# Performance work log

Hardware: AMD Instinct MI355X
Metric: run time of the kernel (lower is better)

Reference implementation:

```python
import jax, jax.numpy as jnp
import numpy as np

N, E, D = 100000, 640000, 128  # nodes, edges, feature dim (in_dim == out_dim == 128)
BN_EPS = 1e-5


def setup_inputs() -> dict:
    key = jax.random.key(0)
    ks = jax.random.split(key, 8)
    x = jax.random.normal(ks[0], (N, D), dtype=jnp.float32)
    edge_index = jax.random.randint(ks[1], (2, E), 0, N, dtype=jnp.int64)
    s = 1.0 / np.sqrt(D)
    W1 = jax.random.uniform(ks[2], (D, D), jnp.float32, -s, s)
    b1 = jax.random.uniform(ks[3], (D,), jnp.float32, -s, s)
    W2 = jax.random.uniform(ks[4], (D, D), jnp.float32, -s, s)
    b2 = jax.random.uniform(ks[5], (D,), jnp.float32, -s, s)
    return {
        "x": x,
        "edge_index": edge_index,
        "eps": jnp.array([0.1], dtype=jnp.float32),
        "W1": W1, "b1": b1,
        "g1": jnp.ones((D,), jnp.float32), "beta1": jnp.zeros((D,), jnp.float32),
        "W2": W2, "b2": b2,
        "g2": jnp.ones((D,), jnp.float32), "beta2": jnp.zeros((D,), jnp.float32),
    }


def _batchnorm(h, gamma, beta):
    # BatchNorm1d in training mode: biased batch stats over the node dim
    mean = jnp.mean(h, axis=0)
    var = jnp.var(h, axis=0)
    return gamma * (h - mean) * jax.lax.rsqrt(var + BN_EPS) + beta


def reference(x, edge_index, eps, W1, b1, g1, beta1, W2, b2, g2, beta2):
    src, dst = edge_index[0], edge_index[1]
    # gather messages from source nodes, scatter-add into destination nodes
    aggr = jax.ops.segment_sum(x[src], dst, num_segments=x.shape[0])  # [N, D]
    h = (1.0 + eps) * x + aggr
    h = jax.nn.relu(_batchnorm(h @ W1.T + b1, g1, beta1))
    h = jax.nn.relu(_batchnorm(h @ W2.T + b2, g2, beta2))
    return h
```

## Files before the change

kernel.cpp:

```cpp
#include <hip/hip_runtime.h>

#define NN 100000
#define DD 128
#define EE 640000
#define NPAD 100352

typedef __bf16 bf16x8 __attribute__((ext_vector_type(8)));
typedef float floatx4 __attribute__((ext_vector_type(4)));

__device__ __forceinline__ unsigned short f2bf(float f) {
    unsigned int u = __float_as_uint(f);
    u += 0x7FFF + ((u >> 16) & 1);
    return (unsigned short)(u >> 16);
}

__global__ __launch_bounds__(256) void hist_k(const int* __restrict__ ei,
                                              int* __restrict__ deg) {
    int e = blockIdx.x * 256 + threadIdx.x;
    if (e < EE) atomicAdd(&deg[ei[EE + e]], 1);
}

__global__ __launch_bounds__(256) void scan1_k(const int* __restrict__ deg,
                                               int* __restrict__ exc,
                                               int* __restrict__ chunkSums) {
    __shared__ int s[256];
    int t = threadIdx.x, g = blockIdx.x * 256 + t;
    int v = (g < NN) ? deg[g] : 0;
    s[t] = v;
    __syncthreads();
    for (int off = 1; off < 256; off <<= 1) {
        int u = (t >= off) ? s[t - off] : 0;
        __syncthreads();
        s[t] += u;
        __syncthreads();
    }
    if (g < NN) exc[g] = s[t] - v;
    if (t == 255) chunkSums[blockIdx.x] = s[255];
}

__global__ __launch_bounds__(512) void scan2_k(int* __restrict__ chunkSums, int n) {
    __shared__ int s[512];
    int t = threadIdx.x;
    int v = (t < n) ? chunkSums[t] : 0;
    s[t] = v;
    __syncthreads();
    for (int off = 1; off < 512; off <<= 1) {
        int u = (t >= off) ? s[t - off] : 0;
        __syncthreads();
        s[t] += u;
        __syncthreads();
    }
    if (t < n) chunkSums[t] = s[t] - v;
}

__global__ __launch_bounds__(256) void scan3_k(int* __restrict__ exc,
                                               const int* __restrict__ chunkSums,
                                               int* __restrict__ cursor) {
    int g = blockIdx.x * 256 + threadIdx.x;
    if (g < NN) {
        int o = exc[g] + chunkSums[blockIdx.x];
        exc[g] = o;
        cursor[g] = o;
    }
}

__global__ __launch_bounds__(256) void esort_k(const int* __restrict__ ei,
                                               int* __restrict__ cursor,
                                               int* __restrict__ ssrc) {
    int e = blockIdx.x * 256 + threadIdx.x;
    if (e >= EE) return;
    int pos = atomicAdd(&cursor[ei[EE + e]], 1);
    ssrc[pos] = ei[e];
}

__global__ __launch_bounds__(256) void aggregate_k(
    const float4* __restrict__ x4, const int* __restrict__ ssrc,
    const int* __restrict__ offs, const int* __restrict__ deg,
    const float* __restrict__ epsp, ushort4* __restrict__ hout) {
    int tid = blockIdx.x * 256 + threadIdx.x;
    int node = tid >> 5, lane = tid & 31;
    if (node >= NN) return;
    int start = offs[node], d = deg[node];
    float ef = 1.0f + epsp[0];
    float4 v = x4[node * 32 + lane];
    float ax = ef * v.x, ay = ef * v.y, az = ef * v.z, aw = ef * v.w;
    for (int j = 0; j < d; j += 4) {
        int r = d - j;
        int b = start + j;
        int s0 = ssrc[b];
        int s1 = ssrc[b + ((r > 1) ? 1 : 0)];
        int s2 = ssrc[b + ((r > 2) ? 2 : 0)];
        int s3 = ssrc[b + ((r > 3) ? 3 : 0)];
        float4 xa = x4[s0 * 32 + lane];
        float4 xb = x4[s1 * 32 + lane];
        float4 xc = x4[s2 * 32 + lane];
        float4 xd = x4[s3 * 32 + lane];
        float m1 = (r > 1) ? 1.f : 0.f;
        float m2 = (r > 2) ? 1.f : 0.f;
        float m3 = (r > 3) ? 1.f : 0.f;
        ax += xa.x; ay += xa.y; az += xa.z; aw += xa.w;
        ax += m1 * xb.x; ay += m1 * xb.y; az += m1 * xb.z; aw += m1 * xb.w;
        ax += m2 * xc.x; ay += m2 * xc.y; az += m2 * xc.z; aw += m2 * xc.w;
        ax += m3 * xd.x; ay += m3 * xd.y; az += m3 * xd.z; aw += m3 * xd.w;
    }
    ushort4 u;
    u.x = f2bf(ax); u.y = f2bf(ay); u.z = f2bf(az); u.w = f2bf(aw);
    hout[node * 32 + lane] = u;
}

template <int FUSE_BN>
__global__ __launch_bounds__(256, 2) void gin_gemm_k(
    const unsigned short* __restrict__ hin,
    const float* __restrict__ yin,
    const float* __restrict__ statsIn,
    const float* __restrict__ gmm,
    const float* __restrict__ bta,
    const float* __restrict__ W, const float* __restrict__ bias,
    float* __restrict__ y, float* __restrict__ statsOut) {
    __shared__ __align__(16) unsigned short Ah[128][136];
    __shared__ __align__(16) unsigned short Bw[128][136];
    __shared__ __align__(16) float s_sum[128];
    __shared__ __align__(16) float s_sq[128];
    __shared__ __align__(16) float sc[128];
    __shared__ __align__(16) float sh[128];

    const int tid = threadIdx.x;
    const int rowBase = blockIdx.x * 128;

    if (tid < 128) {
        s_sum[tid] = 0.f;
        s_sq[tid] = 0.f;
        if (FUSE_BN) {
            const float inv = 1.0f / (float)NN;
            float mean = statsIn[tid] * inv;
            float var = statsIn[128 + tid] * inv - mean * mean;
            float s = gmm[tid] * rsqrtf(var + 1e-5f);
            sc[tid] = s;
            sh[tid] = bta[tid] - mean * s;
        }
    }

    const float4* W4 = (const float4*)W;
#pragma unroll
    for (int j = 0; j < 16; ++j) {
        int f4 = j * 256 + tid;
        int row = f4 >> 5, k4 = f4 & 31;
        float4 wv = W4[f4];
        ushort4 u;
        u.x = f2bf(wv.x); u.y = f2bf(wv.y); u.z = f2bf(wv.z); u.w = f2bf(wv.w);
        *(ushort4*)&Bw[row][k4 * 4] = u;
    }

    if (FUSE_BN) {
        __syncthreads();
        const float4* y4in = (const float4*)yin;
#pragma unroll
        for (int j = 0; j < 16; ++j) {
            int c = j * 256 + tid;
            int row = c >> 5, c4 = c & 31;
            int rg = rowBase + row;
            ushort4 u = make_ushort4(0, 0, 0, 0);
            if (rg < NN) {
                float4 v = y4in[rg * 32 + c4];
                float4 s4 = ((const float4*)sc)[c4];
                float4 b4 = ((const float4*)sh)[c4];
                u.x = f2bf(fmaxf(v.x * s4.x + b4.x, 0.f));
                u.y = f2bf(fmaxf(v.y * s4.y + b4.y, 0.f));
                u.z = f2bf(fmaxf(v.z * s4.z + b4.z, 0.f));
                u.w = f2bf(fmaxf(v.w * s4.w + b4.w, 0.f));
            }
            *(ushort4*)&Ah[row][c4 * 4] = u;
        }
    } else {
        const int4* h16 = (const int4*)hin;
#pragma unroll
        for (int j = 0; j < 8; ++j) {
            int c = j * 256 + tid;
            int row = c >> 4, c8 = c & 15;
            int rg = rowBase + row;
            int4 v = make_int4(0, 0, 0, 0);
            if (rg < NN) v = h16[rg * 16 + c8];
            *(int4*)&Ah[row][c8 * 8] = v;
        }
    }

    __syncthreads();

    const int l = tid & 63, w = tid >> 6;
    const int m = l & 15, q = l >> 4;

    floatx4 acc[2][8];
#pragma unroll
    for (int rt = 0; rt < 2; ++rt)
#pragma unroll
        for (int ct = 0; ct < 8; ++ct) acc[rt][ct] = (floatx4)0.0f;

#pragma unroll
    for (int kc = 0; kc < 4; ++kc) {
        int k0 = kc * 32 + q * 8;
        bf16x8 a0 = *(const bf16x8*)&Ah[w * 32 + m][k0];
        bf16x8 a1 = *(const bf16x8*)&Ah[w * 32 + 16 + m][k0];
#pragma unroll
        for (int ct = 0; ct < 8; ++ct) {
            bf16x8 b = *(const bf16x8*)&Bw[ct * 16 + m][k0];
            acc[0][ct] = __builtin_amdgcn_mfma_f32_16x16x32_bf16(a0, b, acc[0][ct], 0, 0, 0);
            acc[1][ct] = __builtin_amdgcn_mfma_f32_16x16x32_bf16(a1, b, acc[1][ct], 0, 0, 0);
        }
    }

#pragma unroll
    for (int ct = 0; ct < 8; ++ct) {
        int col = ct * 16 + m;
        float bc = bias[col];
        float ps = 0.f, pq = 0.f;
#pragma unroll
        for (int rt = 0; rt < 2; ++rt) {
#pragma unroll
            for (int i = 0; i < 4; ++i) {
                int rg = rowBase + w * 32 + rt * 16 + q * 4 + i;
                if (rg < NN) {
                    float yv = acc[rt][ct][i] + bc;
                    y[rg * 128 + col] = yv;
                    ps += yv;
                    pq += yv * yv;
                }
            }
        }
        atomicAdd(&s_sum[col], ps);
        atomicAdd(&s_sq[col], pq);
    }
    __syncthreads();
    if (tid < 128) {
        unsafeAtomicAdd(&statsOut[tid], s_sum[tid]);
        unsafeAtomicAdd(&statsOut[128 + tid], s_sq[tid]);
    }
}

template <int OUT_BF16>
__global__ __launch_bounds__(256) void bn_relu_k(
    const float* __restrict__ y, const float* __restrict__ stats,
    const float* __restrict__ g, const float* __restrict__ beta,
    float* outf, unsigned short* __restrict__ outh) {
    __shared__ __align__(16) float sc[128];
    __shared__ __align__(16) float sh[128];
    int t = threadIdx.x;
    if (t < 128) {
        const float inv = 1.0f / (float)NN;
        float mean = stats[t] * inv;
        float var = stats[128 + t] * inv - mean * mean;
        float s = g[t] * rsqrtf(var + 1e-5f);
        sc[t] = s;
        sh[t] = beta[t] - mean * s;
    }
    __syncthreads();
    const int total4 = NN * 32;
    const float4* y4 = (const float4*)y;
    for (int i = blockIdx.x * 256 + t; i < total4; i += gridDim.x * 256) {
        int c4 = i & 31;
        float4 v = y4[i];
        float4 s = ((const float4*)sc)[c4];
        float4 b = ((const float4*)sh)[c4];
        float r0 = fmaxf(v.x * s.x + b.x, 0.f);
        float r1 = fmaxf(v.y * s.y + b.y, 0.f);
        float r2 = fmaxf(v.z * s.z + b.z, 0.f);
        float r3 = fmaxf(v.w * s.w + b.w, 0.f);
        if (OUT_BF16) {
            ushort4 u;
            u.x = f2bf(r0); u.y = f2bf(r1); u.z = f2bf(r2); u.w = f2bf(r3);
            ((ushort4*)outh)[i] = u;
        } else {
            ((float4*)outf)[i] = make_float4(r0, r1, r2, r3);
        }
    }
}

extern "C" void kernel_launch(void* const* d_in, const int* in_sizes, int n_in,
                              void* d_out, int out_size, void* d_ws, size_t ws_size,
                              hipStream_t stream) {
    const float* x   = (const float*)d_in[0];
    const int* ei    = (const int*)d_in[1];
    const float* eps = (const float*)d_in[2];
    const float* W1  = (const float*)d_in[3];
    const float* b1  = (const float*)d_in[4];
    const float* g1  = (const float*)d_in[5];
    const float* be1 = (const float*)d_in[6];
    const float* W2  = (const float*)d_in[7];
    const float* b2  = (const float*)d_in[8];
    const float* g2  = (const float*)d_in[9];
    const float* be2 = (const float*)d_in[10];
    float* out = (float*)d_out;

    int* deg        = (int*)d_ws;
    int* offs       = deg + NPAD;
    int* cursor     = offs + NPAD;
    int* chunkSums  = cursor + NPAD;
    int* ssrc       = chunkSums + 512;
    unsigned short* hbuf = (unsigned short*)(ssrc + EE + 256);
    float* stats    = (float*)(hbuf + (size_t)NN * DD);
    float* ybuf     = stats + 512;
    size_t need     = (size_t)((char*)(ybuf + (size_t)NN * DD) - (char*)d_ws);
    const bool fused = ws_size >= need;

    hipMemsetAsync(deg, 0, NPAD * sizeof(int), stream);
    hipMemsetAsync(stats, 0, 512 * sizeof(float), stream);

    const int numChunks = (NN + 255) / 256;
    hist_k<<<(EE + 255) / 256, 256, 0, stream>>>(ei, deg);
    scan1_k<<<numChunks, 256, 0, stream>>>(deg, offs, chunkSums);
    scan2_k<<<1, 512, 0, stream>>>(chunkSums, numChunks);
    scan3_k<<<numChunks, 256, 0, stream>>>(offs, chunkSums, cursor);
    esort_k<<<(EE + 255) / 256, 256, 0, stream>>>(ei, cursor, ssrc);
    aggregate_k<<<(NN * 32 + 255) / 256, 256, 0, stream>>>(
        (const float4*)x, ssrc, offs, deg, eps, (ushort4*)hbuf);

    int gblocks = (NN + 127) / 128;
    if (fused) {
        gin_gemm_k<0><<<gblocks, 256, 0, stream>>>(
            hbuf, nullptr, nullptr, nullptr, nullptr, W1, b1, ybuf, stats);
        gin_gemm_k<1><<<gblocks, 256, 0, stream>>>(
            nullptr, ybuf, stats, g1, be1, W2, b2, out, stats + 256);
        bn_relu_k<0><<<4096, 256, 0, stream>>>(out, stats + 256, g2, be2, out, nullptr);
    } else {
        gin_gemm_k<0><<<gblocks, 256, 0, stream>>>(
            hbuf, nullptr, nullptr, nullptr, nullptr, W1, b1, out, stats);
        bn_relu_k<1><<<4096, 256, 0, stream>>>(out, stats, g1, be1, nullptr, hbuf);
        gin_gemm_k<0><<<gblocks, 256, 0, stream>>>(
            hbuf, nullptr, nullptr, nullptr, nullptr, W2, b2, out, stats + 256);
        bn_relu_k<0><<<4096, 256, 0, stream>>>(out, stats + 256, g2, be2, out, nullptr);
    }
}
```

Before: 345.1 us.

## Load GEMM operands straight to registers and pre-convert weights to bf16

Removes the LDS staging of A and W tiles in the GIN GEMM. Each wave now loads its MFMA A fragments directly from global memory, fusing the BN+ReLU of the previous layer for the second GEMM. It reads pre-converted bf16 weights from global/L2 per column tile. A small kernel converts W1/W2 to bf16 once, instead of every block converting them. Dropping the large shared arrays lets occupancy rise to 4 blocks per CU, and the workspace is reorganised so ybuf overlays the no-longer-needed CSR buffers. The cost is redundant global/L2 reads of weights across waves and uncoalesced row-fragment loads.

```diff
diff --git a/kernel.cpp b/kernel.cpp
--- a/kernel.cpp
+++ b/kernel.cpp
@@ -7,6 +7,12 @@
 
 typedef __bf16 bf16x8 __attribute__((ext_vector_type(8)));
 typedef float floatx4 __attribute__((ext_vector_type(4)));
+
+union BF8 {
+    bf16x8 v;
+    unsigned short u[8];
+    int4 i4;
+};
 
 __device__ __forceinline__ unsigned short f2bf(float f) {
     unsigned int u = __float_as_uint(f);
@@ -71,6 +77,17 @@
     if (e >= EE) return;
     int pos = atomicAdd(&cursor[ei[EE + e]], 1);
     ssrc[pos] = ei[e];
+}
+
+__global__ __launch_bounds__(256) void wconv_k(const float* __restrict__ W1,
+                                               const float* __restrict__ W2,
+                                               unsigned short* __restrict__ wb) {
+    int i = blockIdx.x * 256 + threadIdx.x;
+    const float4* s4 = (i < 4096) ? (const float4*)W1 : (const float4*)W2;
+    float4 v = s4[i & 4095];
+    ushort4 u;
+    u.x = f2bf(v.x); u.y = f2bf(v.y); u.z = f2bf(v.z); u.w = f2bf(v.w);
+    ((ushort4*)wb)[i] = u;
 }
 
 __global__ __launch_bounds__(256) void aggregate_k(
@@ -109,16 +126,14 @@
 }
 
 template <int FUSE_BN>
-__global__ __launch_bounds__(256, 2) void gin_gemm_k(
+__global__ __launch_bounds__(256, 4) void gin_gemm_k(
     const unsigned short* __restrict__ hin,
     const float* __restrict__ yin,
     const float* __restrict__ statsIn,
     const float* __restrict__ gmm,
     const float* __restrict__ bta,
-    const float* __restrict__ W, const float* __restrict__ bias,
+    const unsigned short* __restrict__ Wbf, const float* __restrict__ bias,
     float* __restrict__ y, float* __restrict__ statsOut) {
-    __shared__ __align__(16) unsigned short Ah[128][136];
-    __shared__ __align__(16) unsigned short Bw[128][136];
     __shared__ __align__(16) float s_sum[128];
     __shared__ __align__(16) float s_sq[128];
     __shared__ __align__(16) float sc[128];
@@ -126,6 +141,8 @@
 
     const int tid = threadIdx.x;
     const int rowBase = blockIdx.x * 128;
+    const int l = tid & 63, w = tid >> 6;
+    const int m = l & 15, q = l >> 4;
 
     if (tid < 128) {
         s_sum[tid] = 0.f;
@@ -139,55 +156,49 @@
             sh[tid] = bta[tid] - mean * s;
         }
     }
-
-    const float4* W4 = (const float4*)W;
-#pragma unroll
-    for (int j = 0; j < 16; ++j) {
-        int f4 = j * 256 + tid;
-        int row = f4 >> 5, k4 = f4 & 31;
-        float4 wv = W4[f4];
-        ushort4 u;
-        u.x = f2bf(wv.x); u.y = f2bf(wv.y); u.z = f2bf(wv.z); u.w = f2bf(wv.w);
-        *(ushort4*)&Bw[row][k4 * 4] = u;
-    }
-
-    if (FUSE_BN) {
-        __syncthreads();
-        const float4* y4in = (const float4*)yin;
-#pragma unroll
-        for (int j = 0; j < 16; ++j) {
-            int c = j * 256 + tid;
-            int row = c >> 5, c4 = c & 31;
-            int rg = rowBase + row;
-            ushort4 u = make_ushort4(0, 0, 0, 0);
-            if (rg < NN) {
-                float4 v = y4in[rg * 32 + c4];
-                float4 s4 = ((const float4*)sc)[c4];
-                float4 b4 = ((const float4*)sh)[c4];
-                u.x = f2bf(fmaxf(v.x * s4.x + b4.x, 0.f));
-                u.y = f2bf(fmaxf(v.y * s4.y + b4.y, 0.f));
-                u.z = f2bf(fmaxf(v.z * s4.z + b4.z, 0.f));
-                u.w = f2bf(fmaxf(v.w * s4.w + b4.w, 0.f));
+    __syncthreads();
+
+    bf16x8 a[2][4];
+#pragma unroll
+    for (int rt = 0; rt < 2; ++rt) {
+        int rg = rowBase + w * 32 + rt * 16 + m;
+        bool ok = rg < NN;
+        if (FUSE_BN) {
+            const float* yr = yin + (size_t)rg * 128;
+#pragma unroll
+            for (int kc = 0; kc < 4; ++kc) {
+                int k0 = kc * 32 + q * 8;
+                float4 v0 = make_float4(0.f, 0.f, 0.f, 0.f), v1 = v0;
+                if (ok) {
+                    v0 = *(const float4*)(yr + k0);
+                    v1 = *(const float4*)(yr + k0 + 4);
+                }
+                float4 s0 = *(const float4*)(sc + k0);
+                float4 s1 = *(const float4*)(sc + k0 + 4);
+                float4 h0 = *(const float4*)(sh + k0);
+                float4 h1 = *(const float4*)(sh + k0 + 4);
+                BF8 t;
+                t.u[0] = f2bf(fmaxf(v0.x * s0.x + h0.x, 0.f));
+                t.u[1] = f2bf(fmaxf(v0.y * s0.y + h0.y, 0.f));
+                t.u[2] = f2bf(fmaxf(v0.z * s0.z + h0.z, 0.f));
+                t.u[3] = f2bf(fmaxf(v0.w * s0.w + h0.w, 0.f));
+                t.u[4] = f2bf(fmaxf(v1.x * s1.x + h1.x, 0.f));
+                t.u[5] = f2bf(fmaxf(v1.y * s1.y + h1.y, 0.f));
+                t.u[6] = f2bf(fmaxf(v1.z * s1.z + h1.z, 0.f));
+                t.u[7] = f2bf(fmaxf(v1.w * s1.w + h1.w, 0.f));
+                a[rt][kc] = t.v;
             }
-            *(ushort4*)&Ah[row][c4 * 4] = u;
-        }
-    } else {
-        const int4* h16 = (const int4*)hin;
-#pragma unroll
-        for (int j = 0; j < 8; ++j) {
-            int c = j * 256 + tid;
-            int row = c >> 4, c8 = c & 15;
-            int rg = rowBase + row;
-            int4 v = make_int4(0, 0, 0, 0);
-            if (rg < NN) v = h16[rg * 16 + c8];
-            *(int4*)&Ah[row][c8 * 8] = v;
-        }
-    }
-
-    __syncthreads();
-
-    const int l = tid & 63, w = tid >> 6;
-    const int m = l & 15, q = l >> 4;
+        } else {
+            const unsigned short* ar = hin + (size_t)rg * 128;
+#pragma unroll
+            for (int kc = 0; kc < 4; ++kc) {
+                BF8 t;
+                if (ok) t.i4 = *(const int4*)(ar + kc * 32 + q * 8);
+                else    t.i4 = make_int4(0, 0, 0, 0);
+                a[rt][kc] = t.v;
+            }
+        }
+    }
 
     floatx4 acc[2][8];
 #pragma unroll
@@ -196,15 +207,14 @@
         for (int ct = 0; ct < 8; ++ct) acc[rt][ct] = (floatx4)0.0f;
 
 #pragma unroll
-    for (int kc = 0; kc < 4; ++kc) {
-        int k0 = kc * 32 + q * 8;
-        bf16x8 a0 = *(const bf16x8*)&Ah[w * 32 + m][k0];
-        bf16x8 a1 = *(const bf16x8*)&Ah[w * 32 + 16 + m][k0];
-#pragma unroll
-        for (int ct = 0; ct < 8; ++ct) {
-            bf16x8 b = *(const bf16x8*)&Bw[ct * 16 + m][k0];
-            acc[0][ct] = __builtin_amdgcn_mfma_f32_16x16x32_bf16(a0, b, acc[0][ct], 0, 0, 0);
-            acc[1][ct] = __builtin_amdgcn_mfma_f32_16x16x32_bf16(a1, b, acc[1][ct], 0, 0, 0);
+    for (int ct = 0; ct < 8; ++ct) {
+        const unsigned short* wr = Wbf + (size_t)(ct * 16 + m) * 128;
+#pragma unroll
+        for (int kc = 0; kc < 4; ++kc) {
+            BF8 t;
+            t.i4 = *(const int4*)(wr + kc * 32 + q * 8);
+            acc[0][ct] = __builtin_amdgcn_mfma_f32_16x16x32_bf16(a[0][kc], t.v, acc[0][ct], 0, 0, 0);
+            acc[1][ct] = __builtin_amdgcn_mfma_f32_16x16x32_bf16(a[1][kc], t.v, acc[1][ct], 0, 0, 0);
         }
     }
 
@@ -290,16 +300,24 @@
     const float* be2 = (const float*)d_in[10];
     float* out = (float*)d_out;
 
+    const size_t csr_bytes  = ((size_t)3 * NPAD + 512 + EE + 256) * 4;
+    const size_t ybuf_bytes = (size_t)NN * DD * 4;
+    const size_t hbuf_bytes = (size_t)NN * DD * 2;
+    const size_t fused_need = ybuf_bytes + hbuf_bytes + 2048 + 65536;
+    const bool fused = ws_size >= fused_need;
+
     int* deg        = (int*)d_ws;
     int* offs       = deg + NPAD;
     int* cursor     = offs + NPAD;
     int* chunkSums  = cursor + NPAD;
     int* ssrc       = chunkSums + 512;
-    unsigned short* hbuf = (unsigned short*)(ssrc + EE + 256);
-    float* stats    = (float*)(hbuf + (size_t)NN * DD);
-    float* ybuf     = stats + 512;
-    size_t need     = (size_t)((char*)(ybuf + (size_t)NN * DD) - (char*)d_ws);
-    const bool fused = ws_size >= need;
+    float* ybuf     = (float*)d_ws;
+
+    char* hstart = (char*)d_ws + (fused ? ybuf_bytes : csr_bytes);
+    unsigned short* hbuf = (unsigned short*)hstart;
+    float* stats = (float*)(hstart + hbuf_bytes);
+    unsigned short* wbf = fused ? (unsigned short*)(stats + 512)
+                                : (unsigned short*)deg;
 
     hipMemsetAsync(deg, 0, NPAD * sizeof(int), stream);
     hipMemsetAsync(stats, 0, 512 * sizeof(float), stream);
@@ -312,20 +330,21 @@
     esort_k<<<(EE + 255) / 256, 256, 0, stream>>>(ei, cursor, ssrc);
     aggregate_k<<<(NN * 32 + 255) / 256, 256, 0, stream>>>(
         (const float4*)x, ssrc, offs, deg, eps, (ushort4*)hbuf);
+    wconv_k<<<32, 256, 0, stream>>>(W1, W2, wbf);
 
     int gblocks = (NN + 127) / 128;
     if (fused) {
         gin_gemm_k<0><<<gblocks, 256, 0, stream>>>(
-            hbuf, nullptr, nullptr, nullptr, nullptr, W1, b1, ybuf, stats);
+            hbuf, nullptr, nullptr, nullptr, nullptr, wbf, b1, ybuf, stats);
         gin_gemm_k<1><<<gblocks, 256, 0, stream>>>(
-            nullptr, ybuf, stats, g1, be1, W2, b2, out, stats + 256);
+            nullptr, ybuf, stats, g1, be1, wbf + 16384, b2, out, stats + 256);
         bn_relu_k<0><<<4096, 256, 0, stream>>>(out, stats + 256, g2, be2, out, nullptr);
     } else {
         gin_gemm_k<0><<<gblocks, 256, 0, stream>>>(
-            hbuf, nullptr, nullptr, nullptr, nullptr, W1, b1, out, stats);
+            hbuf, nullptr, nullptr, nullptr, nullptr, wbf, b1, out, stats);
         bn_relu_k<1><<<4096, 256, 0, stream>>>(out, stats, g1, be1, nullptr, hbuf);
         gin_gemm_k<0><<<gblocks, 256, 0, stream>>>(
-            hbuf, nullptr, nullptr, nullptr, nullptr, W2, b2, out, stats + 256);
+            hbuf, nullptr, nullptr, nullptr, nullptr, wbf + 16384, b2, out, stats + 256);
         bn_relu_k<0><<<4096, 256, 0, stream>>>(out, stats + 256, g2, be2, out, nullptr);
     }
 }
```

Result: slower. 355.4 us (+3.0%).
